# Optimization experiments

Hardware: AMD Instinct MI355X
Metric: run time of the kernel (lower is better)

The kernel has to match this reference:

```python
import jax, jax.numpy as jnp
import numpy as np

# dims
B = 4          # videos
F = 8          # frames (space_f)
P = 196        # patches per frame (time_n)
D = 768        # embed dim
H = 12         # heads
HD = D // H    # head dim
L = 4          # blocks
MLP = 4 * D
SCALE = HD ** -0.5
N = 1 + F * P  # sequence length with CLS


def setup_inputs() -> dict:
    key = jax.random.key(0)
    ks = jax.random.split(key, 20)
    s = 0.02
    w = lambda k, shape: (jax.random.normal(k, shape, jnp.float32) * s)
    inp = {
        'x': jax.random.normal(ks[0], (B, N, D), jnp.float32),
        # time attention params (stacked over layers); qkv_bias=False
        'qkv_w_t': w(ks[1], (L, 3 * D, D)),
        'proj_w_t': w(ks[2], (L, D, D)),
        'proj_b_t': jnp.zeros((L, D), jnp.float32),
        # space attention params
        'qkv_w_s': w(ks[3], (L, 3 * D, D)),
        'proj_w_s': w(ks[4], (L, D, D)),
        'proj_b_s': jnp.zeros((L, D), jnp.float32),
        # mlp
        'fc1_w': w(ks[5], (L, MLP, D)),
        'fc1_b': jnp.zeros((L, MLP), jnp.float32),
        'fc2_w': w(ks[6], (L, D, MLP)),
        'fc2_b': jnp.zeros((L, D), jnp.float32),
        # layernorms
        'ln1_g': jnp.ones((L, D), jnp.float32), 'ln1_b': jnp.zeros((L, D), jnp.float32),
        'ln2_g': jnp.ones((L, D), jnp.float32), 'ln2_b': jnp.zeros((L, D), jnp.float32),
        'ln3_g': jnp.ones((L, D), jnp.float32), 'ln3_b': jnp.zeros((L, D), jnp.float32),
    }
    return inp


def _ln(x, g, b):
    m = jnp.mean(x, axis=-1, keepdims=True)
    v = jnp.var(x, axis=-1, keepdims=True)
    return (x - m) * jax.lax.rsqrt(v + 1e-5) * g + b


def _attn(q, k, v):
    sim = jnp.einsum('bid,bjd->bij', q, k)
    a = jax.nn.softmax(sim, axis=-1)
    return jnp.einsum('bij,bjd->bid', a, v)


def _var_attn(x, qkv_w, proj_w, proj_b, mode):
    # x: [B, N, D]; mode in {'space','time'}
    qkv = x @ qkv_w.T                       # [B, N, 3D]
    q, k, v = jnp.split(qkv, 3, axis=-1)
    heads = lambda t: t.reshape(B, N, H, HD).transpose(0, 2, 1, 3).reshape(B * H, N, HD)
    q = heads(q) * SCALE
    k = heads(k)
    v = heads(v)
    cls_q, q_ = q[:, :1], q[:, 1:]
    cls_k, k_ = k[:, :1], k[:, 1:]
    cls_v, v_ = v[:, :1], v[:, 1:]
    # cls token attends over full sequence
    cls_out = _attn(cls_q, k, v)            # [(B h), 1, HD]
    BH = B * H
    if mode == 'space':
        # 'b (f n) d -> (b f) n d'
        split = lambda t: t.reshape(BH * F, P, HD)
        r, g, inner = F, F, P
    else:
        # 'b (f n) d -> (b n) f d'
        split = lambda t: t.reshape(BH, F, P, HD).transpose(0, 2, 1, 3).reshape(BH * P, F, HD)
        r, g, inner = P, P, F
    q_, k_, v_ = split(q_), split(k_), split(v_)
    # broadcast cls k/v across grouped batches: 'b () d -> (b r) () d'
    cls_k_r = jnp.repeat(cls_k, r, axis=0)
    cls_v_r = jnp.repeat(cls_v, r, axis=0)
    k_ = jnp.concatenate([cls_k_r, k_], axis=1)
    v_ = jnp.concatenate([cls_v_r, v_], axis=1)
    out = _attn(q_, k_, v_)                 # [(BH g), inner, HD]
    if mode == 'space':
        out = out.reshape(BH, F * P, HD)
    else:
        out = out.reshape(BH, P, F, HD).transpose(0, 2, 1, 3).reshape(BH, F * P, HD)
    out = jnp.concatenate([cls_out, out], axis=1)          # [(B h), N, HD]
    out = out.reshape(B, H, N, HD).transpose(0, 2, 1, 3).reshape(B, N, D)
    return out @ proj_w.T + proj_b


def _block(x, p):
    a = _ln(x, p['ln3_g'], p['ln3_b'])
    time_out = _var_attn(a, p['qkv_w_t'], p['proj_w_t'], p['proj_b_t'], 'time')
    time_residual = x + time_out
    space_out = _var_attn(_ln(time_residual, p['ln1_g'], p['ln1_b']),
                          p['qkv_w_s'], p['proj_w_s'], p['proj_b_s'], 'space')
    space_residual = x + space_out          # note: residual from original x (frozen-in-time style)
    h = _ln(space_residual, p['ln2_g'], p['ln2_b'])
    h = jax.nn.gelu(h @ p['fc1_w'].T + p['fc1_b'], approximate=False)
    h = h @ p['fc2_w'].T + p['fc2_b']
    return space_residual + h


def reference(x, qkv_w_t, proj_w_t, proj_b_t, qkv_w_s, proj_w_s, proj_b_s,
              fc1_w, fc1_b, fc2_w, fc2_b,
              ln1_g, ln1_b, ln2_g, ln2_b, ln3_g, ln3_b):
    params = dict(qkv_w_t=qkv_w_t, proj_w_t=proj_w_t, proj_b_t=proj_b_t,
                  qkv_w_s=qkv_w_s, proj_w_s=proj_w_s, proj_b_s=proj_b_s,
                  fc1_w=fc1_w, fc1_b=fc1_b, fc2_w=fc2_w, fc2_b=fc2_b,
                  ln1_g=ln1_g, ln1_b=ln1_b, ln2_g=ln2_g, ln2_b=ln2_b,
                  ln3_g=ln3_g, ln3_b=ln3_b)
    def step(carry, layer):
        return _block(carry, layer), None
    out, _ = jax.lax.scan(step, x, params)
    return out
```

## Files before the change

### kernel.cpp

```cpp
#include <hip/hip_runtime.h>
#include <cmath>

#define B_ 4
#define F_ 8
#define P_ 196
#define D_ 768
#define H_ 12
#define HD_ 64
#define L_ 4
#define MLP_ 3072
#define N_ (1 + F_*P_)
#define BN_ (B_*N_)
#define SCALE_ 0.125f
#define QKVC_ (3*D_)

typedef __bf16 bf16x8 __attribute__((ext_vector_type(8)));
typedef float f32x4 __attribute__((ext_vector_type(4)));
typedef const __attribute__((address_space(1))) void* gas_ptr;
typedef __attribute__((address_space(3))) void* las_ptr;

__device__ __forceinline__ unsigned short f2bf(float f) {
  union { __bf16 b; unsigned short u; } cv;
  cv.b = (__bf16)f;
  return cv.u;
}
__device__ __forceinline__ float bf2f(unsigned short u) {
  union { float f; unsigned int i; } cv; cv.i = ((unsigned int)u) << 16; return cv.f;
}
__device__ __forceinline__ unsigned int pk2(float a, float b) {
  return (unsigned int)f2bf(a) | ((unsigned int)f2bf(b) << 16);
}

__device__ __forceinline__ float gelu_exact(float x) {
  return 0.5f * x * (1.0f + erff(x * 0.70710678118654752f));
}

#define SQKV 1769472
#define SPROJ 589824
#define SFC 2359296

__device__ __forceinline__ void cvt_seg(const float* __restrict__ src,
                                        unsigned short* __restrict__ dst,
                                        int n, int t0, int stride) {
  for (int i = t0; i < (n >> 2); i += stride) {
    float4 v = ((const float4*)src)[i];
    ushort4 o;
    o.x = f2bf(v.x); o.y = f2bf(v.y); o.z = f2bf(v.z); o.w = f2bf(v.w);
    ((ushort4*)dst)[i] = o;
  }
}

__global__ __launch_bounds__(256) void cvt_layer_kernel(const float* qt, const float* pt,
                                                        const float* qs, const float* ps,
                                                        const float* f1, const float* f2,
                                                        unsigned short* wb) {
  int t0 = blockIdx.x * blockDim.x + threadIdx.x;
  int stride = gridDim.x * blockDim.x;
  cvt_seg(qt, wb + 0,       SQKV,  t0, stride);
  cvt_seg(pt, wb + 1769472, SPROJ, t0, stride);
  cvt_seg(qs, wb + 2359296, SQKV,  t0, stride);
  cvt_seg(ps, wb + 4128768, SPROJ, t0, stride);
  cvt_seg(f1, wb + 4718592, SFC,   t0, stride);
  cvt_seg(f2, wb + 7077888, SFC,   t0, stride);
}

__global__ __launch_bounds__(256) void ln_kernel(const float* __restrict__ x,
                                                 const float* __restrict__ g,
                                                 const float* __restrict__ b,
                                                 unsigned short* __restrict__ out) {
  int row = blockIdx.x;
  const float* xr = x + (size_t)row * D_;
  unsigned short* orow = out + (size_t)row * D_;
  int tid = threadIdx.x;
  float v0 = xr[tid], v1 = xr[tid + 256], v2 = xr[tid + 512];
  float s  = v0 + v1 + v2;
  float ss = v0*v0 + v1*v1 + v2*v2;
  #pragma unroll
  for (int o = 32; o > 0; o >>= 1) { s += __shfl_xor(s, o); ss += __shfl_xor(ss, o); }
  __shared__ float sm[8];
  int w = tid >> 6;
  if ((tid & 63) == 0) { sm[w*2] = s; sm[w*2+1] = ss; }
  __syncthreads();
  float tot  = sm[0] + sm[2] + sm[4] + sm[6];
  float tot2 = sm[1] + sm[3] + sm[5] + sm[7];
  float mean = tot * (1.0f/D_);
  float var  = tot2 * (1.0f/D_) - mean*mean;
  float rs   = rsqrtf(var + 1e-5f);
  orow[tid]       = f2bf((v0 - mean)*rs*g[tid]       + b[tid]);
  orow[tid + 256] = f2bf((v1 - mean)*rs*g[tid + 256] + b[tid + 256]);
  orow[tid + 512] = f2bf((v2 - mean)*rs*g[tid + 512] + b[tid + 512]);
}

template<int EPI>
__global__ __launch_bounds__(256, 3) void mfma_gemmP(const unsigned short* __restrict__ A,
                                                     const unsigned short* __restrict__ W,
                                                     const float* __restrict__ bias,
                                                     const float* __restrict__ Res,
                                                     void* __restrict__ Cout,
                                                     int M, int NN, int K) {
  __shared__ __align__(16) unsigned short LdsRaw[2*3*128*32];
  unsigned short* LdsA = LdsRaw;
  unsigned short* LdsB = LdsRaw + 3*128*32;
  int tid = threadIdx.x;
  int w = tid >> 6, l = tid & 63;
  int fr = l & 15, fq = l >> 4;
  int wr = w >> 1, wc = w & 1;
  int gx = (M + 127) >> 7;
  int gy = (NN + 127) >> 7;

  int nwg = gridDim.x;
  int orig = blockIdx.x;
  int q8 = nwg >> 3, r8 = nwg & 7;
  int xcd = orig & 7, idx = orig >> 3;
  int wg = (xcd < r8 ? xcd*(q8+1) : r8*(q8+1) + (xcd-r8)*q8) + idx;
  const int GROUPM = 8;
  int npg = GROUPM * gy;
  int gid = wg / npg;
  int first_m = gid * GROUPM;
  int gsz = gx - first_m; if (gsz > GROUPM) gsz = GROUPM;
  int rem = wg - gid * npg;
  int pid_m = first_m + rem % gsz;
  int pid_n = rem / gsz;
  int m0 = pid_m * 128, n0 = pid_n * 128;

  const char* aSrc[2]; const char* bSrc[2];
  #pragma unroll
  for (int q = 0; q < 2; ++q) {
    int c = q*256 + tid;
    int row = c >> 2;
    int cb = ((c & 3) << 4) ^ (((row >> 1) & 3) << 4);
    int ra = m0 + row; if (ra >= M) ra = M - 1;
    aSrc[q] = (const char*)A + ((size_t)ra * K) * 2 + cb;
    bSrc[q] = (const char*)W + ((size_t)(n0 + row) * K) * 2 + cb;
  }

  f32x4 acc[4][4] = {};
  int nt = K >> 5;
  int lswz = ((fr >> 1) & 3) << 4;

#define STAGEP(buf, kt) do { int kb_ = (kt) * 64;                                                                      \
    __builtin_amdgcn_global_load_lds((gas_ptr)(aSrc[0]+kb_), (las_ptr)(&LdsA[(buf)*4096 + (0*256 + w*64)*8]), 16, 0, 0); \
    __builtin_amdgcn_global_load_lds((gas_ptr)(aSrc[1]+kb_), (las_ptr)(&LdsA[(buf)*4096 + (1*256 + w*64)*8]), 16, 0, 0); \
    __builtin_amdgcn_global_load_lds((gas_ptr)(bSrc[0]+kb_), (las_ptr)(&LdsB[(buf)*4096 + (0*256 + w*64)*8]), 16, 0, 0); \
    __builtin_amdgcn_global_load_lds((gas_ptr)(bSrc[1]+kb_), (las_ptr)(&LdsB[(buf)*4096 + (1*256 + w*64)*8]), 16, 0, 0); \
  } while (0)

  STAGEP(0, 0);
  STAGEP(1, 1);
  int cur = 0;
  for (int t = 0; t < nt; ++t) {
    if (t + 1 < nt) {
      asm volatile("s_waitcnt vmcnt(4)" ::: "memory");
    } else {
      asm volatile("s_waitcnt vmcnt(0)" ::: "memory");
    }
    __builtin_amdgcn_s_barrier();
    const char* bufA = (const char*)(LdsA + cur*4096);
    const char* bufB = (const char*)(LdsB + cur*4096);
    bf16x8 afrag[4], bfrag[4];
    #pragma unroll
    for (int n = 0; n < 4; ++n)
      bfrag[n] = *(const bf16x8*)(bufB + (wc*64 + n*16 + fr)*64 + ((fq*16) ^ lswz));
    #pragma unroll
    for (int m = 0; m < 4; ++m)
      afrag[m] = *(const bf16x8*)(bufA + (wr*64 + m*16 + fr)*64 + ((fq*16) ^ lswz));
    #pragma unroll
    for (int m = 0; m < 4; ++m)
      #pragma unroll
      for (int n = 0; n < 4; ++n)
        acc[m][n] = __builtin_amdgcn_mfma_f32_16x16x32_bf16(afrag[m], bfrag[n], acc[m][n], 0, 0, 0);
    if (t + 2 < nt) {
      int nb = cur + 2; if (nb >= 3) nb -= 3;
      STAGEP(nb, t + 2);
    }
    ++cur; if (cur == 3) cur = 0;
  }
#undef STAGEP

  float* eps = (float*)LdsRaw;
  #pragma unroll
  for (int h = 0; h < 2; ++h) {
    __syncthreads();
    if (wr == h) {
      #pragma unroll
      for (int n = 0; n < 4; ++n)
        #pragma unroll
        for (int i = 0; i < 4; ++i)
          #pragma unroll
          for (int r = 0; r < 4; ++r) {
            int lrow = i*16 + fq*4 + r;
            int col  = wc*64 + n*16 + fr;
            eps[lrow*128 + (col ^ (((lrow >> 2) & 7) << 2))] = acc[i][n][r];
          }
    }
    __syncthreads();
    #pragma unroll
    for (int p = 0; p < 8; ++p) {
      int idx = p*256 + tid;
      int lrow = idx >> 5, cg = idx & 31;
      int col0 = cg * 4;
      int grow = m0 + h*64 + lrow;
      if (grow < M) {
        f32x4 v = *(const f32x4*)&eps[lrow*128 + (col0 ^ (((lrow >> 2) & 7) << 2))];
        int gcol = n0 + col0;
        if (EPI == 1 || EPI == 2) {
          float4 bv = *(const float4*)&bias[gcol];
          v[0] += bv.x; v[1] += bv.y; v[2] += bv.z; v[3] += bv.w;
        }
        if (EPI == 1) {
          float4 rv = *(const float4*)&Res[(size_t)grow * NN + gcol];
          v[0] += rv.x; v[1] += rv.y; v[2] += rv.z; v[3] += rv.w;
          *(float4*)&((float*)Cout)[(size_t)grow * NN + gcol] = make_float4(v[0], v[1], v[2], v[3]);
        } else if (EPI == 0) {
          *(float4*)&((float*)Cout)[(size_t)grow * NN + gcol] = make_float4(v[0], v[1], v[2], v[3]);
        } else {
          if (EPI == 2) {
            v[0] = gelu_exact(v[0]); v[1] = gelu_exact(v[1]);
            v[2] = gelu_exact(v[2]); v[3] = gelu_exact(v[3]);
          }
          unsigned long long ov = (unsigned long long)pk2(v[0], v[1])
                                | ((unsigned long long)pk2(v[2], v[3]) << 32);
          *(unsigned long long*)&((unsigned short*)Cout)[(size_t)grow * NN + gcol] = ov;
        }
      }
    }
  }
}

#define CLS_CH 7
#define CLS_CHSZ 256
__global__ __launch_bounds__(256) void cls_attn_part(const unsigned short* __restrict__ qkv,
                                                     float* __restrict__ part) {
  int blk = blockIdx.x;
  int c = blk % CLS_CH, bh = blk / CLS_CH;
  int b = bh / H_, h = bh % H_;
  const unsigned short* base = qkv + (size_t)b * N_ * QKVC_ + h * HD_;
  __shared__ float q[HD_];
  __shared__ float s[CLS_CHSZ];
  __shared__ float redm[4], redd[4];
  __shared__ float pvs[4][HD_];
  int tid = threadIdx.x;
  if (tid < HD_) q[tid] = bf2f(base[tid]) * SCALE_;
  __syncthreads();
  int j = c * CLS_CHSZ + tid;
  float sc = -1e30f;
  if (j < N_) {
    const unsigned short* kp = base + (size_t)j * QKVC_ + D_;
    float acc = 0.f;
    #pragma unroll
    for (int cc = 0; cc < 8; ++cc) {
      uint4 kv = *(const uint4*)(kp + cc*8);
      const unsigned short* e = (const unsigned short*)&kv;
      #pragma unroll
      for (int t = 0; t < 8; ++t) acc = fmaf(q[cc*8+t], bf2f(e[t]), acc);
    }
    sc = acc;
  }
  float m = sc;
  #pragma unroll
  for (int o = 32; o > 0; o >>= 1) m = fmaxf(m, __shfl_xor(m, o));
  if ((tid & 63) == 0) redm[tid >> 6] = m;
  __syncthreads();
  m = fmaxf(fmaxf(redm[0], redm[1]), fmaxf(redm[2], redm[3]));
  float p = (j < N_) ? __expf(sc - m) : 0.f;
  s[tid] = p;
  float den = p;
  #pragma unroll
  for (int o = 32; o > 0; o >>= 1) den += __shfl_xor(den, o);
  if ((tid & 63) == 0) redd[tid >> 6] = den;
  __syncthreads();
  float dtot = redd[0] + redd[1] + redd[2] + redd[3];
  int lane = tid & 63, g = tid >> 6;
  float acc = 0.f;
  #pragma unroll 8
  for (int i = 0; i < CLS_CHSZ/4; ++i) {
    int jl = g + 4*i;
    int jj = c * CLS_CHSZ + jl;
    if (jj < N_) acc = fmaf(s[jl], bf2f(base[(size_t)jj * QKVC_ + 2*D_ + lane]), acc);
  }
  pvs[g][lane] = acc;
  __syncthreads();
  if (g == 0) {
    float pv = pvs[0][lane] + pvs[1][lane] + pvs[2][lane] + pvs[3][lane];
    float* pp = part + ((size_t)bh * CLS_CH + c) * 66;
    if (lane == 0) { pp[0] = m; pp[1] = dtot; }
    pp[2 + lane] = pv;
  }
}

__global__ __launch_bounds__(64) void cls_attn_reduce(const float* __restrict__ part,
                                                      unsigned short* __restrict__ att) {
  int bh = blockIdx.x;
  int b = bh / H_, h = bh % H_;
  int lane = threadIdx.x;
  const float* pp = part + (size_t)bh * CLS_CH * 66;
  float m = -1e30f;
  #pragma unroll
  for (int c = 0; c < CLS_CH; ++c) m = fmaxf(m, pp[c*66]);
  float den = 0.f, acc = 0.f;
  #pragma unroll
  for (int c = 0; c < CLS_CH; ++c) {
    float wfac = __expf(pp[c*66] - m);
    den += pp[c*66 + 1] * wfac;
    acc += pp[c*66 + 2 + lane] * wfac;
  }
  att[(size_t)(b * N_) * D_ + h * HD_ + lane] = f2bf(acc / den);
}

__global__ __launch_bounds__(256) void space_attn_mfma(const unsigned short* __restrict__ qkv,
                                                       unsigned short* __restrict__ att) {
  int blk = blockIdx.x;
  int f = blk % F_; int bh = blk / F_;
  int b = bh / H_, h = bh % H_;
  const unsigned short* qbase = qkv + (size_t)b * N_ * QKVC_ + h * HD_;
  __shared__ __align__(16) unsigned short Ksm[208*64];
  __shared__ __align__(16) unsigned short Vtm[64*256];
  __shared__ __align__(16) unsigned short Pm[4*16*256];
  int tid = threadIdx.x;

  for (int c = tid; c < 208*8; c += 256) {
    int j = c >> 3, cb = (c & 7) * 16;
    uint4 val = make_uint4(0,0,0,0);
    if (j < 197) {
      int n = (j == 0) ? 0 : (1 + f*P_ + j - 1);
      val = *(const uint4*)(qbase + (size_t)n*QKVC_ + D_ + cb/2);
    }
    *(uint4*)((char*)Ksm + j*128 + (cb ^ ((j&7)<<4))) = val;
  }
  for (int c = tid; c < 112*8; c += 256) {
    int jj = c % 112, dc = c / 112;
    int j0 = jj * 2;
    uint4 r0 = make_uint4(0,0,0,0), r1 = make_uint4(0,0,0,0);
    if (j0 < 197) {
      int n = (j0 == 0) ? 0 : (1 + f*P_ + j0 - 1);
      r0 = *(const uint4*)(qbase + (size_t)n*QKVC_ + 2*D_ + dc*8);
    }
    if (j0 + 1 < 197) {
      int n = 1 + f*P_ + j0;
      r1 = *(const uint4*)(qbase + (size_t)n*QKVC_ + 2*D_ + dc*8);
    }
    const unsigned short* e0 = (const unsigned short*)&r0;
    const unsigned short* e1 = (const unsigned short*)&r1;
    #pragma unroll
    for (int e = 0; e < 8; ++e) {
      int d = dc*8 + e;
      unsigned int pk = (unsigned int)e0[e] | ((unsigned int)e1[e] << 16);
      *(unsigned int*)((char*)Vtm + d*512 + ((2*j0) ^ ((d&7)<<4))) = pk;
    }
  }
  int w = tid >> 6, l = tid & 63;
  int fr = l & 15, fq = l >> 4;
  char* Pw = (char*)Pm + w * 8192;
  {
    int q = l >> 2, cb = 416 + (l & 3) * 8;
    *(unsigned long long*)(Pw + q*512 + (cb ^ ((q&7)<<4))) = 0ull;
  }
  __syncthreads();

  int swz = (fr & 7) << 4;
  for (int qt = w; qt <= 12; qt += 4) {
    int qrow = qt*16 + fr; if (qrow > 195) qrow = 195;
    int n_q = 1 + f*P_ + qrow;
    bf16x8 qf0 = *(const bf16x8*)(qbase + (size_t)n_q*QKVC_ + fq*8);
    bf16x8 qf1 = *(const bf16x8*)(qbase + (size_t)n_q*QKVC_ + 32 + fq*8);
    f32x4 s[13];
    #pragma unroll
    for (int jt = 0; jt < 13; ++jt) s[jt] = (f32x4){0.f,0.f,0.f,0.f};
    #pragma unroll
    for (int jt = 0; jt < 13; ++jt) {
      bf16x8 a0 = *(const bf16x8*)((char*)Ksm + (jt*16+fr)*128 + ((fq*16) ^ swz));
      s[jt] = __builtin_amdgcn_mfma_f32_16x16x32_bf16(a0, qf0, s[jt], 0, 0, 0);
      bf16x8 a1 = *(const bf16x8*)((char*)Ksm + (jt*16+fr)*128 + ((64 + fq*16) ^ swz));
      s[jt] = __builtin_amdgcn_mfma_f32_16x16x32_bf16(a1, qf1, s[jt], 0, 0, 0);
    }
    float m = -1e30f;
    #pragma unroll
    for (int jt = 0; jt < 13; ++jt) {
      #pragma unroll
      for (int r = 0; r < 4; ++r) {
        if (jt*16 + fq*4 + r < 197) m = fmaxf(m, s[jt][r]);
      }
    }
    m = fmaxf(m, __shfl_xor(m, 16));
    m = fmaxf(m, __shfl_xor(m, 32));
    float den = 0.f;
    #pragma unroll
    for (int jt = 0; jt < 13; ++jt) {
      #pragma unroll
      for (int r = 0; r < 4; ++r) {
        float p = (jt*16 + fq*4 + r < 197) ? __expf((s[jt][r] - m) * SCALE_) : 0.f;
        s[jt][r] = p;
        den += p;
      }
    }
    den += __shfl_xor(den, 16);
    den += __shfl_xor(den, 32);
    #pragma unroll
    for (int jt = 0; jt < 13; ++jt) {
      unsigned long long pv = (unsigned long long)pk2(s[jt][0], s[jt][1])
                            | ((unsigned long long)pk2(s[jt][2], s[jt][3]) << 32);
      *(unsigned long long*)(Pw + fr*512 + ((jt*32 + fq*8) ^ swz)) = pv;
    }
    float rden = 1.0f / den;
    bool wr_ok = (qt*16 + fr) < 196;
    int n_out = 1 + f*P_ + qt*16 + fr;
    #pragma unroll
    for (int dt = 0; dt < 4; ++dt) {
      f32x4 o = (f32x4){0.f,0.f,0.f,0.f};
      #pragma unroll
      for (int ks = 0; ks < 7; ++ks) {
        bf16x8 av = *(const bf16x8*)((char*)Vtm + (dt*16+fr)*512 + ((ks*64 + fq*16) ^ swz));
        bf16x8 bp = *(const bf16x8*)(Pw + fr*512 + ((ks*64 + fq*16) ^ swz));
        o = __builtin_amdgcn_mfma_f32_16x16x32_bf16(av, bp, o, 0, 0, 0);
      }
      if (wr_ok) {
        unsigned long long ov = (unsigned long long)pk2(o[0]*rden, o[1]*rden)
                              | ((unsigned long long)pk2(o[2]*rden, o[3]*rden) << 32);
        *(unsigned long long*)(att + (size_t)(b*N_ + n_out)*D_ + h*HD_ + dt*16 + fq*4) = ov;
      }
    }
  }
}

__global__ __launch_bounds__(256) void time_attn_kernel(const unsigned short* __restrict__ qkv,
                                                        unsigned short* __restrict__ att) {
  int idx = blockIdx.x * 4 + (threadIdx.x >> 6);
  int bh = idx / P_, p = idx % P_;
  int b = bh / H_, h = bh % H_;
  int lane = threadIdx.x & 63;
  const unsigned short* base = qkv + (size_t)b * N_ * QKVC_ + h * HD_ + lane;
  float k[9], v[9];
  k[0] = bf2f(base[D_]);
  v[0] = bf2f(base[2*D_]);
  #pragma unroll
  for (int j = 0; j < 8; ++j) {
    size_t r = (size_t)(1 + j * P_ + p) * QKVC_;
    k[j+1] = bf2f(base[r + D_]);
    v[j+1] = bf2f(base[r + 2*D_]);
  }
  #pragma unroll 1
  for (int f = 0; f < F_; ++f) {
    size_t qr = (size_t)(1 + f * P_ + p) * QKVC_;
    float qd = bf2f(base[qr]) * SCALE_;
    float s[9];
    #pragma unroll
    for (int j = 0; j < 9; ++j) {
      float prod = qd * k[j];
      #pragma unroll
      for (int o = 32; o > 0; o >>= 1) prod += __shfl_xor(prod, o);
      s[j] = prod;
    }
    float m = s[0];
    #pragma unroll
    for (int j = 1; j < 9; ++j) m = fmaxf(m, s[j]);
    float den = 0.f, o_ = 0.f;
    #pragma unroll
    for (int j = 0; j < 9; ++j) {
      float pj = __expf(s[j] - m);
      den += pj;
      o_ = fmaf(pj, v[j], o_);
    }
    att[(size_t)(b * N_ + 1 + f * P_ + p) * D_ + h * HD_ + lane] = f2bf(o_ / den);
  }
}

extern "C" void kernel_launch(void* const* d_in, const int* in_sizes, int n_in,
                              void* d_out, int out_size, void* d_ws, size_t ws_size,
                              hipStream_t stream) {
  const float* x_in     = (const float*)d_in[0];
  const float* qkv_w_t  = (const float*)d_in[1];
  const float* proj_w_t = (const float*)d_in[2];
  const float* proj_b_t = (const float*)d_in[3];
  const float* qkv_w_s  = (const float*)d_in[4];
  const float* proj_w_s = (const float*)d_in[5];
  const float* proj_b_s = (const float*)d_in[6];
  const float* fc1_w    = (const float*)d_in[7];
  const float* fc1_b    = (const float*)d_in[8];
  const float* fc2_w    = (const float*)d_in[9];
  const float* fc2_b    = (const float*)d_in[10];
  const float* ln1_g    = (const float*)d_in[11];
  const float* ln1_b    = (const float*)d_in[12];
  const float* ln2_g    = (const float*)d_in[13];
  const float* ln2_b    = (const float*)d_in[14];
  const float* ln3_g    = (const float*)d_in[15];
  const float* ln3_b    = (const float*)d_in[16];

  float* X_out = (float*)d_out;
  char* ws = (char*)d_ws;
  unsigned short* Wbf = (unsigned short*)ws;
  const size_t WOFF = 18874368;
  unsigned short* QKVbf = (unsigned short*)(ws + WOFF);
  unsigned short* Hbf   = (unsigned short*)(ws + WOFF);
  float*          TR    = (float*)(ws + WOFF + 57839616);
  unsigned short* Abf   = (unsigned short*)(ws + WOFF + 57839616 + 19279872);
  float*          CLSP  = (float*)(ws + WOFF + 57839616 + 19279872 + 9639936);

  unsigned short* wqkv_t = Wbf + 0;
  unsigned short* wproj_t= Wbf + 1769472;
  unsigned short* wqkv_s = Wbf + 2359296;
  unsigned short* wproj_s= Wbf + 4128768;
  unsigned short* wfc1   = Wbf + 4718592;
  unsigned short* wfc2   = Wbf + 7077888;

  dim3 blk(256);
  dim3 g_qkv(50 * 18), g_proj(50 * 6), g_fc1(50 * 24), g_fc2(50 * 6);

  for (int l = 0; l < L_; ++l) {
    const float* X = (l == 0) ? x_in : (const float*)X_out;
    cvt_layer_kernel<<<2048, blk, 0, stream>>>(
        qkv_w_t + (size_t)l*SQKV, proj_w_t + (size_t)l*SPROJ,
        qkv_w_s + (size_t)l*SQKV, proj_w_s + (size_t)l*SPROJ,
        fc1_w + (size_t)l*SFC, fc2_w + (size_t)l*SFC, Wbf);
    ln_kernel<<<BN_, blk, 0, stream>>>(X, ln3_g + l*D_, ln3_b + l*D_, Abf);
    mfma_gemmP<3><<<g_qkv, blk, 0, stream>>>(Abf, wqkv_t, nullptr, nullptr, QKVbf, BN_, QKVC_, D_);
    cls_attn_part<<<B_*H_*CLS_CH, blk, 0, stream>>>(QKVbf, CLSP);
    cls_attn_reduce<<<B_*H_, dim3(64), 0, stream>>>(CLSP, Abf);
    time_attn_kernel<<<(B_*H_*P_)/4, blk, 0, stream>>>(QKVbf, Abf);
    mfma_gemmP<1><<<g_proj, blk, 0, stream>>>(Abf, wproj_t, proj_b_t + l*D_, X, TR, BN_, D_, D_);
    ln_kernel<<<BN_, blk, 0, stream>>>(TR, ln1_g + l*D_, ln1_b + l*D_, Abf);
    mfma_gemmP<3><<<g_qkv, blk, 0, stream>>>(Abf, wqkv_s, nullptr, nullptr, QKVbf, BN_, QKVC_, D_);
    cls_attn_part<<<B_*H_*CLS_CH, blk, 0, stream>>>(QKVbf, CLSP);
    cls_attn_reduce<<<B_*H_, dim3(64), 0, stream>>>(CLSP, Abf);
    space_attn_mfma<<<B_*H_*F_, blk, 0, stream>>>(QKVbf, Abf);
    mfma_gemmP<1><<<g_proj, blk, 0, stream>>>(Abf, wproj_s, proj_b_s + l*D_, X, TR, BN_, D_, D_);
    ln_kernel<<<BN_, blk, 0, stream>>>(TR, ln2_g + l*D_, ln2_b + l*D_, Abf);
    mfma_gemmP<2><<<g_fc1, blk, 0, stream>>>(Abf, wfc1, fc1_b + l*MLP_, nullptr, Hbf, BN_, MLP_, D_);
    mfma_gemmP<1><<<g_fc2, blk, 0, stream>>>(Hbf, wfc2, fc2_b + l*D_, TR, X_out, BN_, D_, MLP_);
  }
}
```

Baseline: 1.561 ms.

## Add 256x128-tile triple-buffered GEMM for QKV and FC1 projections

```diff
diff --git a/kernel.cpp b/kernel.cpp
--- a/kernel.cpp
+++ b/kernel.cpp
@@ -227,6 +227,151 @@
   }
 }
 
+template<int EPI>
+__global__ __launch_bounds__(256, 2) void mfma_gemmW(const unsigned short* __restrict__ A,
+                                                     const unsigned short* __restrict__ W,
+                                                     const float* __restrict__ bias,
+                                                     const float* __restrict__ Res,
+                                                     void* __restrict__ Cout,
+                                                     int M, int NN, int K) {
+  __shared__ __align__(16) unsigned short LdsRaw[3*256*32 + 3*128*32];
+  unsigned short* LdsA = LdsRaw;
+  unsigned short* LdsB = LdsRaw + 3*256*32;
+  int tid = threadIdx.x;
+  int w = tid >> 6, l = tid & 63;
+  int fr = l & 15, fq = l >> 4;
+  int wr = w >> 1, wc = w & 1;
+  int gx = (M + 255) >> 8;
+  int gy = (NN + 127) >> 7;
+
+  int nwg = gridDim.x;
+  int orig = blockIdx.x;
+  int q8 = nwg >> 3, r8 = nwg & 7;
+  int xcd = orig & 7, idx = orig >> 3;
+  int wg = (xcd < r8 ? xcd*(q8+1) : r8*(q8+1) + (xcd-r8)*q8) + idx;
+  const int GROUPM = 4;
+  int npg = GROUPM * gy;
+  int gid = wg / npg;
+  int first_m = gid * GROUPM;
+  int gsz = gx - first_m; if (gsz > GROUPM) gsz = GROUPM;
+  int rem = wg - gid * npg;
+  int pid_m = first_m + rem % gsz;
+  int pid_n = rem / gsz;
+  int m0 = pid_m * 256, n0 = pid_n * 128;
+
+  const char* aSrc[4]; const char* bSrc[2];
+  #pragma unroll
+  for (int q = 0; q < 4; ++q) {
+    int c = q*256 + tid;
+    int row = c >> 2;
+    int cb = ((c & 3) << 4) ^ (((row >> 1) & 3) << 4);
+    int ra = m0 + row; if (ra >= M) ra = M - 1;
+    aSrc[q] = (const char*)A + ((size_t)ra * K) * 2 + cb;
+  }
+  #pragma unroll
+  for (int q = 0; q < 2; ++q) {
+    int c = q*256 + tid;
+    int row = c >> 2;
+    int cb = ((c & 3) << 4) ^ (((row >> 1) & 3) << 4);
+    bSrc[q] = (const char*)W + ((size_t)(n0 + row) * K) * 2 + cb;
+  }
+
+  f32x4 acc[8][4] = {};
+  int nt = K >> 5;
+  int lswz = ((fr >> 1) & 3) << 4;
+
+#define STAGEW(buf, kt) do { int kb_ = (kt) * 64;                                                                      \
+    __builtin_amdgcn_global_load_lds((gas_ptr)(aSrc[0]+kb_), (las_ptr)(&LdsA[(buf)*8192 + (0*256 + w*64)*8]), 16, 0, 0); \
+    __builtin_amdgcn_global_load_lds((gas_ptr)(aSrc[1]+kb_), (las_ptr)(&LdsA[(buf)*8192 + (1*256 + w*64)*8]), 16, 0, 0); \
+    __builtin_amdgcn_global_load_lds((gas_ptr)(aSrc[2]+kb_), (las_ptr)(&LdsA[(buf)*8192 + (2*256 + w*64)*8]), 16, 0, 0); \
+    __builtin_amdgcn_global_load_lds((gas_ptr)(aSrc[3]+kb_), (las_ptr)(&LdsA[(buf)*8192 + (3*256 + w*64)*8]), 16, 0, 0); \
+    __builtin_amdgcn_global_load_lds((gas_ptr)(bSrc[0]+kb_), (las_ptr)(&LdsB[(buf)*4096 + (0*256 + w*64)*8]), 16, 0, 0); \
+    __builtin_amdgcn_global_load_lds((gas_ptr)(bSrc[1]+kb_), (las_ptr)(&LdsB[(buf)*4096 + (1*256 + w*64)*8]), 16, 0, 0); \
+  } while (0)
+
+  STAGEW(0, 0);
+  STAGEW(1, 1);
+  int cur = 0;
+  for (int t = 0; t < nt; ++t) {
+    if (t + 1 < nt) {
+      asm volatile("s_waitcnt vmcnt(6)" ::: "memory");
+    } else {
+      asm volatile("s_waitcnt vmcnt(0)" ::: "memory");
+    }
+    __builtin_amdgcn_s_barrier();
+    const char* bufA = (const char*)(LdsA + cur*8192);
+    const char* bufB = (const char*)(LdsB + cur*4096);
+    bf16x8 afrag[8], bfrag[4];
+    #pragma unroll
+    for (int n = 0; n < 4; ++n)
+      bfrag[n] = *(const bf16x8*)(bufB + (wc*64 + n*16 + fr)*64 + ((fq*16) ^ lswz));
+    #pragma unroll
+    for (int m = 0; m < 8; ++m)
+      afrag[m] = *(const bf16x8*)(bufA + (wr*128 + m*16 + fr)*64 + ((fq*16) ^ lswz));
+    #pragma unroll
+    for (int m = 0; m < 8; ++m)
+      #pragma unroll
+      for (int n = 0; n < 4; ++n)
+        acc[m][n] = __builtin_amdgcn_mfma_f32_16x16x32_bf16(afrag[m], bfrag[n], acc[m][n], 0, 0, 0);
+    if (t + 2 < nt) {
+      int nb = cur + 2; if (nb >= 3) nb -= 3;
+      STAGEW(nb, t + 2);
+    }
+    ++cur; if (cur == 3) cur = 0;
+  }
+#undef STAGEW
+
+  float* eps = (float*)LdsRaw;
+  #pragma unroll
+  for (int qh = 0; qh < 4; ++qh) {
+    __syncthreads();
+    if (wr == (qh >> 1)) {
+      int mbase = (qh & 1) * 4;
+      #pragma unroll
+      for (int n = 0; n < 4; ++n)
+        #pragma unroll
+        for (int mi = 0; mi < 4; ++mi)
+          #pragma unroll
+          for (int r = 0; r < 4; ++r) {
+            int lrow = mi*16 + fq*4 + r;
+            int col  = wc*64 + n*16 + fr;
+            eps[lrow*128 + (col ^ (((lrow >> 2) & 7) << 2))] = acc[mbase + mi][n][r];
+          }
+    }
+    __syncthreads();
+    #pragma unroll
+    for (int p = 0; p < 8; ++p) {
+      int idx = p*256 + tid;
+      int lrow = idx >> 5, cg = idx & 31;
+      int col0 = cg * 4;
+      int grow = m0 + qh*64 + lrow;
+      if (grow < M) {
+        f32x4 v = *(const f32x4*)&eps[lrow*128 + (col0 ^ (((lrow >> 2) & 7) << 2))];
+        int gcol = n0 + col0;
+        if (EPI == 1 || EPI == 2) {
+          float4 bv = *(const float4*)&bias[gcol];
+          v[0] += bv.x; v[1] += bv.y; v[2] += bv.z; v[3] += bv.w;
+        }
+        if (EPI == 1) {
+          float4 rv = *(const float4*)&Res[(size_t)grow * NN + gcol];
+          v[0] += rv.x; v[1] += rv.y; v[2] += rv.z; v[3] += rv.w;
+          *(float4*)&((float*)Cout)[(size_t)grow * NN + gcol] = make_float4(v[0], v[1], v[2], v[3]);
+        } else if (EPI == 0) {
+          *(float4*)&((float*)Cout)[(size_t)grow * NN + gcol] = make_float4(v[0], v[1], v[2], v[3]);
+        } else {
+          if (EPI == 2) {
+            v[0] = gelu_exact(v[0]); v[1] = gelu_exact(v[1]);
+            v[2] = gelu_exact(v[2]); v[3] = gelu_exact(v[3]);
+          }
+          unsigned long long ov = (unsigned long long)pk2(v[0], v[1])
+                                | ((unsigned long long)pk2(v[2], v[3]) << 32);
+          *(unsigned long long*)&((unsigned short*)Cout)[(size_t)grow * NN + gcol] = ov;
+        }
+      }
+    }
+  }
+}
+
 #define CLS_CH 7
 #define CLS_CHSZ 256
 __global__ __launch_bounds__(256) void cls_attn_part(const unsigned short* __restrict__ qkv,
@@ -503,7 +648,8 @@
   unsigned short* wfc2   = Wbf + 7077888;
 
   dim3 blk(256);
-  dim3 g_qkv(50 * 18), g_proj(50 * 6), g_fc1(50 * 24), g_fc2(50 * 6);
+  dim3 g_qkv(25 * 18), g_fc1(25 * 24);
+  dim3 g_proj(50 * 6), g_fc2(50 * 6);
 
   for (int l = 0; l < L_; ++l) {
     const float* X = (l == 0) ? x_in : (const float*)X_out;
@@ -512,19 +658,19 @@
         qkv_w_s + (size_t)l*SQKV, proj_w_s + (size_t)l*SPROJ,
         fc1_w + (size_t)l*SFC, fc2_w + (size_t)l*SFC, Wbf);
     ln_kernel<<<BN_, blk, 0, stream>>>(X, ln3_g + l*D_, ln3_b + l*D_, Abf);
-    mfma_gemmP<3><<<g_qkv, blk, 0, stream>>>(Abf, wqkv_t, nullptr, nullptr, QKVbf, BN_, QKVC_, D_);
+    mfma_gemmW<3><<<g_qkv, blk, 0, stream>>>(Abf, wqkv_t, nullptr, nullptr, QKVbf, BN_, QKVC_, D_);
     cls_attn_part<<<B_*H_*CLS_CH, blk, 0, stream>>>(QKVbf, CLSP);
     cls_attn_reduce<<<B_*H_, dim3(64), 0, stream>>>(CLSP, Abf);
     time_attn_kernel<<<(B_*H_*P_)/4, blk, 0, stream>>>(QKVbf, Abf);
     mfma_gemmP<1><<<g_proj, blk, 0, stream>>>(Abf, wproj_t, proj_b_t + l*D_, X, TR, BN_, D_, D_);
     ln_kernel<<<BN_, blk, 0, stream>>>(TR, ln1_g + l*D_, ln1_b + l*D_, Abf);
-    mfma_gemmP<3><<<g_qkv, blk, 0, stream>>>(Abf, wqkv_s, nullptr, nullptr, QKVbf, BN_, QKVC_, D_);
+    mfma_gemmW<3><<<g_qkv, blk, 0, stream>>>(Abf, wqkv_s, nullptr, nullptr, QKVbf, BN_, QKVC_, D_);
     cls_attn_part<<<B_*H_*CLS_CH, blk, 0, stream>>>(QKVbf, CLSP);
     cls_attn_reduce<<<B_*H_, dim3(64), 0, stream>>>(CLSP, Abf);
     space_attn_mfma<<<B_*H_*F_, blk, 0, stream>>>(QKVbf, Abf);
     mfma_gemmP<1><<<g_proj, blk, 0, stream>>>(Abf, wproj_s, proj_b_s + l*D_, X, TR, BN_, D_, D_);
     ln_kernel<<<BN_, blk, 0, stream>>>(TR, ln2_g + l*D_, ln2_b + l*D_, Abf);
-    mfma_gemmP<2><<<g_fc1, blk, 0, stream>>>(Abf, wfc1, fc1_b + l*MLP_, nullptr, Hbf, BN_, MLP_, D_);
+    mfma_gemmW<2><<<g_fc1, blk, 0, stream>>>(Abf, wfc1, fc1_b + l*MLP_, nullptr, Hbf, BN_, MLP_, D_);
     mfma_gemmP<1><<<g_fc2, blk, 0, stream>>>(Hbf, wfc2, fc2_b + l*D_, TR, X_out, BN_, D_, MLP_);
   }
 }
```

Measured after the change: 1.832 ms. +17.3%, slower.
